# Performance work log

Hardware: AMD Instinct MI355X
Metric: run time of the kernel (lower is better)

Reference implementation:

```python
import jax, jax.numpy as jnp
import numpy as np

L, T, E, D, H, B = 2, 8, 2, 128, 128, 32768
NE = T * E  # total experts per layer = 16


def setup_inputs() -> dict:
    key = jax.random.key(0)
    ks = jax.random.split(key, 8)
    s = 1.0 / np.sqrt(D)
    inputs = jax.random.normal(ks[0], (B, T, D), dtype=jnp.float32)
    w1 = jax.random.uniform(ks[1], (L, NE, D, H), jnp.float32, -s, s)
    b1 = jax.random.uniform(ks[2], (L, NE, H), jnp.float32, -s, s)
    w2 = jax.random.uniform(ks[3], (L, NE, H, H), jnp.float32, -s, s)
    b2 = jax.random.uniform(ks[4], (L, NE, H), jnp.float32, -s, s)
    gate_w = jax.random.uniform(ks[5], (L, T, D, NE), jnp.float32, -s, s)
    gate_b = jax.random.uniform(ks[6], (L, T, NE), jnp.float32, -s, s)
    se = 1.0 / np.sqrt(E)
    sew = jax.random.uniform(ks[7], (L, T, E), jnp.float32, -se, se)
    return {"inputs": inputs, "w1": w1, "b1": b1, "w2": w2, "b2": b2,
            "gate_w": gate_w, "gate_b": gate_b, "sew": sew}


def reference(inputs, w1, b1, w2, b2, gate_w, gate_b, sew):
    x = inputs  # [B, T, D]
    for l in range(L):
        # each task's input feeds its num_task_experts experts
        x_exp = jnp.repeat(x, E, axis=1)  # [B, NE, D]
        h = jax.nn.relu(jnp.einsum('bed,edh->beh', x_exp, w1[l]) + b1[l])
        eo = jax.nn.relu(jnp.einsum('beh,eho->beo', h, w2[l]) + b2[l])  # [B, NE, H]
        # per-task gating over all experts
        gates = jax.nn.softmax(jnp.einsum('btd,tde->bte', x, gate_w[l]) + gate_b[l], axis=-1)  # [B, T, NE]
        fused = jnp.einsum('bte,beh->bth', gates, eo)  # [B, T, H]
        # self-expert residual (num_task_experts > 1 branch)
        eo_r = eo.reshape(eo.shape[0], T, E, -1)  # [B, T, E, H]
        fused = fused + jnp.einsum('te,bteh->bth', sew[l], eo_r)
        x = fused
    return x
```

## Files before the change

### kernel.cpp

```cpp
#include <hip/hip_runtime.h>


typedef float f32x4 __attribute__((ext_vector_type(4)));
typedef _Float16 f16;
typedef f16 f16x8 __attribute__((ext_vector_type(8)));
typedef f16 f16x4 __attribute__((ext_vector_type(4)));

#define MFMA(a, b, c) __builtin_amdgcn_mfma_f32_16x16x32_f16(a, b, c, 0, 0, 0)
#define LOSC (1.0f / 2048.0f)

__device__ __forceinline__ void split2h(float f, f16& h, f16& l) {
  h = (f16)f;
  l = (f16)((f - (float)h) * 2048.0f);
}

__global__ __launch_bounds__(256) void kxform(
    const float* __restrict__ w1, const float* __restrict__ w2,
    const float* __restrict__ gw, f16* __restrict__ w1T,
    f16* __restrict__ w2T, f16* __restrict__ gwT) {
  int idx = blockIdx.x * 256 + threadIdx.x;
  if (idx < 131072) {
    const float* src = (idx < 65536) ? w1 : w2;
    f16* dst = (idx < 65536) ? w1T : w2T;
    int i = idx & 65535;
    int lane = i & 63;
    int it = (i >> 6) & 7;
    int ks = (i >> 9) & 3;
    int q = i >> 11;
    int g = lane >> 4, le = lane & 15;
    f16x8 vh;
#pragma unroll
    for (int j = 0; j < 8; ++j)
      vh[j] = (f16)src[((size_t)q * 128 + (32 * ks + 8 * g + j)) * 128 + 16 * it + le];
    *(f16x8*)(dst + (size_t)i * 8) = vh;
  } else {
    int i = idx - 131072;
    if (i >= 4096) return;
    int lane = i & 63;
    int ks = (i >> 6) & 3;
    int q = (i >> 8) & 15;
    int g = lane >> 4, le = lane & 15;
    f16x8 vh, vl;
#pragma unroll
    for (int j = 0; j < 8; ++j) {
      float f = gw[((size_t)q * 128 + (32 * ks + 8 * g + j)) * 16 + le];
      f16 h, l;
      split2h(f, h, l);
      vh[j] = h;
      vl[j] = l;
    }
    *(f16x8*)(gwT + (size_t)i * 8) = vh;
    *(f16x8*)(gwT + 32768 + (size_t)i * 8) = vl;
  }
}

__global__ __launch_bounds__(256, 2) void kexp(
    const float* __restrict__ x0, const f16* __restrict__ x1in,
    const f16* __restrict__ w1T, const f16* __restrict__ w2T,
    const float* __restrict__ b1, const float* __restrict__ b2,
    f16* __restrict__ eo, int layer) {
  __shared__ f16 sX[2][8192];
  __shared__ f16 sH[8192];
  __shared__ f16 sEO[8192];
  const int tid = threadIdx.x;
  const int lane = tid & 63;
  const int it2 = tid >> 6;
  const int g = lane >> 4, le = lane & 15;
  const int e = blockIdx.x & 15;
  const int r0 = (blockIdx.x >> 4) * 1024;
  const int te = e >> 1;
  const int lx = layer * 16 + e;

  f16x8 w1r[2][4], w2r[2][4];
#pragma unroll
  for (int i2 = 0; i2 < 2; ++i2)
#pragma unroll
    for (int ks = 0; ks < 4; ++ks) {
      size_t fb = ((size_t)((lx * 4 + ks) * 8 + 2 * it2 + i2) * 64 + lane) * 8;
      w1r[i2][ks] = *(const f16x8*)(w1T + fb);
      w2r[i2][ks] = *(const f16x8*)(w2T + fb);
    }
  f32x4 b1v[2], b2v[2];
#pragma unroll
  for (int i2 = 0; i2 < 2; ++i2) {
    b1v[i2] = *(const f32x4*)(b1 + lx * 128 + 32 * it2 + 16 * i2 + 4 * g);
    b2v[i2] = *(const f32x4*)(b2 + lx * 128 + 32 * it2 + 16 * i2 + 4 * g);
  }

  const int srow = tid >> 2;
  const int gr = (tid & 3) * 4;
  f16x8 pre[4];
  auto stage_load = [&](int tile) {
    size_t base = ((size_t)(r0 + tile * 64 + srow) * 8 + te) * 128 + gr * 8;
    if (layer == 0) {
#pragma unroll
      for (int q = 0; q < 4; ++q) {
        f32x4 f0 = *(const f32x4*)(x0 + base + q * 8);
        f32x4 f1 = *(const f32x4*)(x0 + base + q * 8 + 4);
#pragma unroll
        for (int z = 0; z < 4; ++z) {
          pre[q][z] = (f16)f0[z];
          pre[q][4 + z] = (f16)f1[z];
        }
      }
    } else {
#pragma unroll
      for (int q = 0; q < 4; ++q)
        pre[q] = *(const f16x8*)(x1in + base + q * 8);
    }
  };
  auto stage_write = [&](int buf) {
#pragma unroll
    for (int q = 0; q < 4; ++q)
      *(f16x8*)(&sX[buf][srow * 128 + 8 * ((gr + q) ^ (srow & 7))]) = pre[q];
  };
  auto eo_flush = [&](int tile) {
#pragma unroll
    for (int i = 0; i < 4; ++i) {
      int slot = i * 256 + tid;
      int row = slot >> 4, c = slot & 15;
      f16x8 v = *(const f16x8*)(&sEO[row * 128 + 8 * (c ^ (row & 7))]);
      *(f16x8*)(eo + ((size_t)(r0 + tile * 64 + row) * 16 + e) * 128 + 8 * c) = v;
    }
  };

  stage_load(0);
  stage_write(0);
  __syncthreads();

  for (int tile = 0; tile < 16; ++tile) {
    const int b = tile & 1;
    if (tile < 15) stage_load(tile + 1);
    if (tile > 0) eo_flush(tile - 1);
    {
      f32x4 a[2][4];
#pragma unroll
      for (int i2 = 0; i2 < 2; ++i2)
#pragma unroll
        for (int j = 0; j < 4; ++j) a[i2][j] = f32x4{0.f, 0.f, 0.f, 0.f};
#pragma unroll
      for (int ks = 0; ks < 4; ++ks)
#pragma unroll
        for (int j = 0; j < 4; ++j) {
          int brow = 16 * j + le;
          f16x8 bf = *(const f16x8*)(&sX[b][brow * 128 + 8 * ((4 * ks + g) ^ (brow & 7))]);
#pragma unroll
          for (int i2 = 0; i2 < 2; ++i2)
            a[i2][j] = MFMA(w1r[i2][ks], bf, a[i2][j]);
        }
#pragma unroll
      for (int i2 = 0; i2 < 2; ++i2)
#pragma unroll
        for (int j = 0; j < 4; ++j) {
          int brow = 16 * j + le;
          f16x4 hv;
#pragma unroll
          for (int r = 0; r < 4; ++r)
            hv[r] = (f16)fmaxf(a[i2][j][r] + b1v[i2][r], 0.f);
          *(f16x4*)(&sH[brow * 128 + 8 * ((4 * it2 + 2 * i2 + (g >> 1)) ^ (brow & 7)) +
                        4 * (g & 1)]) = hv;
        }
    }
    __syncthreads();
    {
      f32x4 a[2][4];
#pragma unroll
      for (int i2 = 0; i2 < 2; ++i2)
#pragma unroll
        for (int j = 0; j < 4; ++j) a[i2][j] = f32x4{0.f, 0.f, 0.f, 0.f};
#pragma unroll
      for (int ks = 0; ks < 4; ++ks)
#pragma unroll
        for (int j = 0; j < 4; ++j) {
          int brow = 16 * j + le;
          f16x8 bf = *(const f16x8*)(&sH[brow * 128 + 8 * ((4 * ks + g) ^ (brow & 7))]);
#pragma unroll
          for (int i2 = 0; i2 < 2; ++i2)
            a[i2][j] = MFMA(w2r[i2][ks], bf, a[i2][j]);
        }
#pragma unroll
      for (int i2 = 0; i2 < 2; ++i2)
#pragma unroll
        for (int j = 0; j < 4; ++j) {
          int brow = 16 * j + le;
          f16x4 ev;
#pragma unroll
          for (int r = 0; r < 4; ++r)
            ev[r] = (f16)fmaxf(a[i2][j][r] + b2v[i2][r], 0.f);
          *(f16x4*)(&sEO[brow * 128 + 8 * ((4 * it2 + 2 * i2 + (g >> 1)) ^ (brow & 7)) +
                         4 * (g & 1)]) = ev;
        }
    }
    if (tile < 15) stage_write(b ^ 1);
#pragma unroll
    for (int i2 = 0; i2 < 2; ++i2)
#pragma unroll
      for (int ks = 0; ks < 4; ++ks) {
        asm volatile("" : "+v"(w1r[i2][ks]));
        asm volatile("" : "+v"(w2r[i2][ks]));
      }
    __syncthreads();
  }
  eo_flush(15);
}

__global__ __launch_bounds__(512, 4) void kmix(
    const float* __restrict__ x0, const f16* __restrict__ x1in,
    const f16* __restrict__ gwT, const float* __restrict__ gb,
    const float* __restrict__ sw, const f16* __restrict__ eo,
    f16* __restrict__ x1out, float* __restrict__ fout, int layer) {
  __shared__ float sG[8 * 16 * 32];
  const int tid = threadIdx.x;
  const int lane = tid & 63;
  const int t = tid >> 6;
  const int g = lane >> 4, le = lane & 15;
  const int r0 = blockIdx.x * 32;
  const int lt = layer * 8 + t;

  {
    f32x4 l1[2], l2[2];
#pragma unroll
    for (int j = 0; j < 2; ++j) {
      l1[j] = f32x4{0.f, 0.f, 0.f, 0.f};
      l2[j] = f32x4{0.f, 0.f, 0.f, 0.f};
    }
#pragma unroll
    for (int ks = 0; ks < 4; ++ks) {
      size_t fb = ((size_t)(lt * 4 + ks) * 64 + lane) * 8;
      f16x8 ah = *(const f16x8*)(gwT + fb);
      f16x8 al = *(const f16x8*)(gwT + 32768 + fb);
#pragma unroll
      for (int j = 0; j < 2; ++j) {
        size_t xoff = ((size_t)(r0 + 16 * j + le) * 8 + t) * 128 + 32 * ks + 8 * g;
        f16x8 bf;
        if (layer == 0) {
          f32x4 f0 = *(const f32x4*)(x0 + xoff);
          f32x4 f1 = *(const f32x4*)(x0 + xoff + 4);
#pragma unroll
          for (int z = 0; z < 4; ++z) {
            bf[z] = (f16)f0[z];
            bf[4 + z] = (f16)f1[z];
          }
        } else {
          bf = *(const f16x8*)(x1in + xoff);
        }
        l1[j] = MFMA(ah, bf, l1[j]);
        l2[j] = MFMA(al, bf, l2[j]);
      }
    }
#pragma unroll
    for (int j = 0; j < 2; ++j) {
      float zb[4];
#pragma unroll
      for (int r = 0; r < 4; ++r)
        zb[r] = l1[j][r] + l2[j][r] * LOSC + gb[lt * 16 + 4 * g + r];
      float m4 = fmaxf(fmaxf(zb[0], zb[1]), fmaxf(zb[2], zb[3]));
      m4 = fmaxf(m4, __shfl_xor(m4, 16, 64));
      m4 = fmaxf(m4, __shfl_xor(m4, 32, 64));
      float p4[4], s4 = 0.f;
#pragma unroll
      for (int r = 0; r < 4; ++r) {
        p4[r] = __expf(zb[r] - m4);
        s4 += p4[r];
      }
      s4 += __shfl_xor(s4, 16, 64);
      s4 += __shfl_xor(s4, 32, 64);
      float inv = 1.f / s4;
#pragma unroll
      for (int r = 0; r < 4; ++r)
        sG[(t * 16 + 4 * g + r) * 32 + 16 * j + le] = p4[r] * inv;
    }
  }
  __syncthreads();

  const int lrow = tid >> 4;
  const int grow = r0 + lrow;
  const int c0 = (tid & 15) * 8;
  f32x4 am[8][2];
#pragma unroll
  for (int tt = 0; tt < 8; ++tt)
#pragma unroll
    for (int k = 0; k < 2; ++k) am[tt][k] = f32x4{0.f, 0.f, 0.f, 0.f};

  for (int ee = 0; ee < 16; ++ee) {
    const int tte = ee >> 1, eh = ee & 1;
    f16x8 ev = *(const f16x8*)(eo + ((size_t)grow * 16 + ee) * 128 + c0);
    float evf[8];
#pragma unroll
    for (int z = 0; z < 8; ++z) evf[z] = (float)ev[z];
    float ssew = sw[(layer * 8 + tte) * 2 + eh];
#pragma unroll
    for (int tt = 0; tt < 8; ++tt) {
      float coef = sG[(tt * 16 + ee) * 32 + lrow] + (tt == tte ? ssew : 0.f);
#pragma unroll
      for (int z = 0; z < 8; ++z)
        am[tt][z >> 2][z & 3] = fmaf(coef, evf[z], am[tt][z >> 2][z & 3]);
    }
  }
#pragma unroll
  for (int tt = 0; tt < 8; ++tt) {
    size_t off = ((size_t)grow * 8 + tt) * 128 + c0;
    if (layer == 0) {
      f16x8 hv;
#pragma unroll
      for (int z = 0; z < 8; ++z) hv[z] = (f16)am[tt][z >> 2][z & 3];
      *(f16x8*)(x1out + off) = hv;
    } else {
      *(f32x4*)(fout + off) = am[tt][0];
      *(f32x4*)(fout + off + 4) = am[tt][1];
    }
  }
}

extern "C" void kernel_launch(void* const* d_in, const int* in_sizes, int n_in,
                              void* d_out, int out_size, void* d_ws, size_t ws_size,
                              hipStream_t stream) {
  const float* x0 = (const float*)d_in[0];
  const float* w1 = (const float*)d_in[1];
  const float* b1 = (const float*)d_in[2];
  const float* w2 = (const float*)d_in[3];
  const float* b2 = (const float*)d_in[4];
  const float* gw = (const float*)d_in[5];
  const float* gb = (const float*)d_in[6];
  const float* sw = (const float*)d_in[7];

  f16* w1T = (f16*)d_ws;
  f16* w2T = (f16*)((char*)d_ws + 1048576);
  f16* gwT = (f16*)((char*)d_ws + 2097152);
  f16* x1h = (f16*)((char*)d_ws + 4194304);
  f16* eo = (f16*)((char*)d_ws + 71303168);
  float* out = (float*)d_out;

  kxform<<<528, 256, 0, stream>>>(w1, w2, gw, w1T, w2T, gwT);

  kexp<<<512, 256, 0, stream>>>(x0, nullptr, w1T, w2T, b1, b2, eo, 0);
  kmix<<<1024, 512, 0, stream>>>(x0, nullptr, gwT, gb, sw, eo, x1h, nullptr, 0);
  kexp<<<512, 256, 0, stream>>>(nullptr, x1h, w1T, w2T, b1, b2, eo, 1);
  kmix<<<1024, 512, 0, stream>>>(nullptr, x1h, gwT, gb, sw, eo, nullptr, out, 1);
}
```

Measured before the change: 290.5 us.

## Process batch in four chunks and store expert outputs expert-major

The batch is split into four chunks of 8192 rows. Both layers' expert and mixing kernels run per chunk, so the fp16 expert-output buffer written by kexp and read by kmix is a quarter the size and more likely to stay in cache between the two kernels. The eo buffer layout changes from row-major-by-expert to expert-major within a chunk. In exchange there are four times as many kernel launches. Each kexp block now processes only 4 tiles, so its register-resident weight loads are spread over less work, and kmix gets fewer blocks per launch, which may underfill the GPU.

```diff
diff --git a/kernel.cpp b/kernel.cpp
--- a/kernel.cpp
+++ b/kernel.cpp
@@ -8,6 +8,7 @@
 
 #define MFMA(a, b, c) __builtin_amdgcn_mfma_f32_16x16x32_f16(a, b, c, 0, 0, 0)
 #define LOSC (1.0f / 2048.0f)
+#define CH 8192
 
 __device__ __forceinline__ void split2h(float f, f16& h, f16& l) {
   h = (f16)f;
@@ -58,7 +59,7 @@
     const float* __restrict__ x0, const f16* __restrict__ x1in,
     const f16* __restrict__ w1T, const f16* __restrict__ w2T,
     const float* __restrict__ b1, const float* __restrict__ b2,
-    f16* __restrict__ eo, int layer) {
+    f16* __restrict__ eo, int layer, int c0) {
   __shared__ f16 sX[2][8192];
   __shared__ f16 sH[8192];
   __shared__ f16 sEO[8192];
@@ -67,7 +68,7 @@
   const int it2 = tid >> 6;
   const int g = lane >> 4, le = lane & 15;
   const int e = blockIdx.x & 15;
-  const int r0 = (blockIdx.x >> 4) * 1024;
+  const int r0l = (blockIdx.x >> 4) * 256;
   const int te = e >> 1;
   const int lx = layer * 16 + e;
 
@@ -91,7 +92,8 @@
   const int gr = (tid & 3) * 4;
   f16x8 pre[4];
   auto stage_load = [&](int tile) {
-    size_t base = ((size_t)(r0 + tile * 64 + srow) * 8 + te) * 128 + gr * 8;
+    size_t base =
+        ((size_t)(c0 + r0l + tile * 64 + srow) * 8 + te) * 128 + gr * 8;
     if (layer == 0) {
 #pragma unroll
       for (int q = 0; q < 4; ++q) {
@@ -120,7 +122,7 @@
       int slot = i * 256 + tid;
       int row = slot >> 4, c = slot & 15;
       f16x8 v = *(const f16x8*)(&sEO[row * 128 + 8 * (c ^ (row & 7))]);
-      *(f16x8*)(eo + ((size_t)(r0 + tile * 64 + row) * 16 + e) * 128 + 8 * c) = v;
+      *(f16x8*)(eo + ((size_t)e * CH + (r0l + tile * 64 + row)) * 128 + 8 * c) = v;
     }
   };
 
@@ -128,9 +130,9 @@
   stage_write(0);
   __syncthreads();
 
-  for (int tile = 0; tile < 16; ++tile) {
+  for (int tile = 0; tile < 4; ++tile) {
     const int b = tile & 1;
-    if (tile < 15) stage_load(tile + 1);
+    if (tile < 3) stage_load(tile + 1);
     if (tile > 0) eo_flush(tile - 1);
     {
       f32x4 a[2][4];
@@ -191,7 +193,7 @@
                          4 * (g & 1)]) = ev;
         }
     }
-    if (tile < 15) stage_write(b ^ 1);
+    if (tile < 3) stage_write(b ^ 1);
 #pragma unroll
     for (int i2 = 0; i2 < 2; ++i2)
 #pragma unroll
@@ -201,20 +203,20 @@
       }
     __syncthreads();
   }
-  eo_flush(15);
+  eo_flush(3);
 }
 
 __global__ __launch_bounds__(512, 4) void kmix(
     const float* __restrict__ x0, const f16* __restrict__ x1in,
     const f16* __restrict__ gwT, const float* __restrict__ gb,
     const float* __restrict__ sw, const f16* __restrict__ eo,
-    f16* __restrict__ x1out, float* __restrict__ fout, int layer) {
+    f16* __restrict__ x1out, float* __restrict__ fout, int layer, int c0) {
   __shared__ float sG[8 * 16 * 32];
   const int tid = threadIdx.x;
   const int lane = tid & 63;
   const int t = tid >> 6;
   const int g = lane >> 4, le = lane & 15;
-  const int r0 = blockIdx.x * 32;
+  const int lr0 = blockIdx.x * 32;
   const int lt = layer * 8 + t;
 
   {
@@ -231,7 +233,8 @@
       f16x8 al = *(const f16x8*)(gwT + 32768 + fb);
 #pragma unroll
       for (int j = 0; j < 2; ++j) {
-        size_t xoff = ((size_t)(r0 + 16 * j + le) * 8 + t) * 128 + 32 * ks + 8 * g;
+        size_t xoff =
+            ((size_t)(c0 + lr0 + 16 * j + le) * 8 + t) * 128 + 32 * ks + 8 * g;
         f16x8 bf;
         if (layer == 0) {
           f32x4 f0 = *(const f32x4*)(x0 + xoff);
@@ -274,8 +277,9 @@
   __syncthreads();
 
   const int lrow = tid >> 4;
-  const int grow = r0 + lrow;
-  const int c0 = (tid & 15) * 8;
+  const int lr = lr0 + lrow;
+  const int grow = c0 + lr;
+  const int cq = (tid & 15) * 8;
   f32x4 am[8][2];
 #pragma unroll
   for (int tt = 0; tt < 8; ++tt)
@@ -284,7 +288,7 @@
 
   for (int ee = 0; ee < 16; ++ee) {
     const int tte = ee >> 1, eh = ee & 1;
-    f16x8 ev = *(const f16x8*)(eo + ((size_t)grow * 16 + ee) * 128 + c0);
+    f16x8 ev = *(const f16x8*)(eo + ((size_t)ee * CH + lr) * 128 + cq);
     float evf[8];
 #pragma unroll
     for (int z = 0; z < 8; ++z) evf[z] = (float)ev[z];
@@ -299,7 +303,7 @@
   }
 #pragma unroll
   for (int tt = 0; tt < 8; ++tt) {
-    size_t off = ((size_t)grow * 8 + tt) * 128 + c0;
+    size_t off = ((size_t)grow * 8 + tt) * 128 + cq;
     if (layer == 0) {
       f16x8 hv;
 #pragma unroll
@@ -333,8 +337,11 @@
 
   kxform<<<528, 256, 0, stream>>>(w1, w2, gw, w1T, w2T, gwT);
 
-  kexp<<<512, 256, 0, stream>>>(x0, nullptr, w1T, w2T, b1, b2, eo, 0);
-  kmix<<<1024, 512, 0, stream>>>(x0, nullptr, gwT, gb, sw, eo, x1h, nullptr, 0);
-  kexp<<<512, 256, 0, stream>>>(nullptr, x1h, w1T, w2T, b1, b2, eo, 1);
-  kmix<<<1024, 512, 0, stream>>>(nullptr, x1h, gwT, gb, sw, eo, nullptr, out, 1);
-}
+  for (int c = 0; c < 4; ++c) {
+    int c0 = c * CH;
+    kexp<<<512, 256, 0, stream>>>(x0, x1h, w1T, w2T, b1, b2, eo, 0, c0);
+    kmix<<<256, 512, 0, stream>>>(x0, x1h, gwT, gb, sw, eo, x1h, out, 0, c0);
+    kexp<<<512, 256, 0, stream>>>(x0, x1h, w1T, w2T, b1, b2, eo, 1, c0);
+    kmix<<<256, 512, 0, stream>>>(x0, x1h, gwT, gb, sw, eo, nullptr, out, 1, c0);
+  }
+}
```

New measurement: 312.0 us. 1.07x slower.

## Pre-cast input to fp16 and stage expert tiles via direct global-to-LDS loads

Applied to the files above, without the earlier changes.

Adds a separate cast kernel that converts the fp32 input to fp16 once, so both layer-0 kernels read half-precision data instead of each converting fp32 on the fly. The expert kernel now fills its shared-memory input tiles with global_load_lds (direct global-to-LDS copies with a swizzled source), which removes the register prefetch buffer and the separate LDS write step. The expert-output buffer layout changes from row-major per batch to per-expert contiguous. The trade-off is an extra pass over the input and a larger workspace footprint.

```diff
diff --git a/kernel.cpp b/kernel.cpp
--- a/kernel.cpp
+++ b/kernel.cpp
@@ -8,10 +8,26 @@
 
 #define MFMA(a, b, c) __builtin_amdgcn_mfma_f32_16x16x32_f16(a, b, c, 0, 0, 0)
 #define LOSC (1.0f / 2048.0f)
+#define AS1 __attribute__((address_space(1)))
+#define AS3 __attribute__((address_space(3)))
 
 __device__ __forceinline__ void split2h(float f, f16& h, f16& l) {
   h = (f16)f;
   l = (f16)((f - (float)h) * 2048.0f);
+}
+
+__global__ __launch_bounds__(256) void kxcast(const float* __restrict__ x0,
+                                              f16* __restrict__ x0h) {
+  size_t i = ((size_t)blockIdx.x * 256 + threadIdx.x) * 8;
+  f32x4 f0 = *(const f32x4*)(x0 + i);
+  f32x4 f1 = *(const f32x4*)(x0 + i + 4);
+  f16x8 v;
+#pragma unroll
+  for (int z = 0; z < 4; ++z) {
+    v[z] = (f16)f0[z];
+    v[4 + z] = (f16)f1[z];
+  }
+  *(f16x8*)(x0h + i) = v;
 }
 
 __global__ __launch_bounds__(256) void kxform(
@@ -55,10 +71,9 @@
 }
 
 __global__ __launch_bounds__(256, 2) void kexp(
-    const float* __restrict__ x0, const f16* __restrict__ x1in,
-    const f16* __restrict__ w1T, const f16* __restrict__ w2T,
-    const float* __restrict__ b1, const float* __restrict__ b2,
-    f16* __restrict__ eo, int layer) {
+    const f16* __restrict__ xs, const f16* __restrict__ w1T,
+    const f16* __restrict__ w2T, const float* __restrict__ b1,
+    const float* __restrict__ b2, f16* __restrict__ eo, int layer) {
   __shared__ f16 sX[2][8192];
   __shared__ f16 sH[8192];
   __shared__ f16 sEO[8192];
@@ -87,32 +102,17 @@
     b2v[i2] = *(const f32x4*)(b2 + lx * 128 + 32 * it2 + 16 * i2 + 4 * g);
   }
 
-  const int srow = tid >> 2;
-  const int gr = (tid & 3) * 4;
-  f16x8 pre[4];
-  auto stage_load = [&](int tile) {
-    size_t base = ((size_t)(r0 + tile * 64 + srow) * 8 + te) * 128 + gr * 8;
-    if (layer == 0) {
-#pragma unroll
-      for (int q = 0; q < 4; ++q) {
-        f32x4 f0 = *(const f32x4*)(x0 + base + q * 8);
-        f32x4 f1 = *(const f32x4*)(x0 + base + q * 8 + 4);
-#pragma unroll
-        for (int z = 0; z < 4; ++z) {
-          pre[q][z] = (f16)f0[z];
-          pre[q][4 + z] = (f16)f1[z];
-        }
-      }
-    } else {
-#pragma unroll
-      for (int q = 0; q < 4; ++q)
-        pre[q] = *(const f16x8*)(x1in + base + q * 8);
-    }
-  };
-  auto stage_write = [&](int buf) {
-#pragma unroll
-    for (int q = 0; q < 4; ++q)
-      *(f16x8*)(&sX[buf][srow * 128 + 8 * ((gr + q) ^ (srow & 7))]) = pre[q];
+  auto stage_gl = [&](int buf, int tile) {
+#pragma unroll
+    for (int i = 0; i < 4; ++i) {
+      int row = 16 * it2 + 4 * i + (lane >> 4);
+      int gc = lane & 15;
+      const f16* src = xs + ((size_t)(r0 + tile * 64 + row) * 8 + te) * 128 +
+                       (gc ^ (row & 7)) * 8;
+      f16* dst = &sX[buf][(16 * it2 + 4 * i) * 128];
+      __builtin_amdgcn_global_load_lds((const AS1 void*)src, (AS3 void*)dst,
+                                       16, 0, 0);
+    }
   };
   auto eo_flush = [&](int tile) {
 #pragma unroll
@@ -120,17 +120,16 @@
       int slot = i * 256 + tid;
       int row = slot >> 4, c = slot & 15;
       f16x8 v = *(const f16x8*)(&sEO[row * 128 + 8 * (c ^ (row & 7))]);
-      *(f16x8*)(eo + ((size_t)(r0 + tile * 64 + row) * 16 + e) * 128 + 8 * c) = v;
+      *(f16x8*)(eo + ((size_t)e * 32768 + (r0 + tile * 64 + row)) * 128 + 8 * c) = v;
     }
   };
 
-  stage_load(0);
-  stage_write(0);
+  stage_gl(0, 0);
   __syncthreads();
 
   for (int tile = 0; tile < 16; ++tile) {
     const int b = tile & 1;
-    if (tile < 15) stage_load(tile + 1);
+    if (tile < 15) stage_gl(b ^ 1, tile + 1);
     if (tile > 0) eo_flush(tile - 1);
     {
       f32x4 a[2][4];
@@ -191,24 +190,16 @@
                          4 * (g & 1)]) = ev;
         }
     }
-    if (tile < 15) stage_write(b ^ 1);
-#pragma unroll
-    for (int i2 = 0; i2 < 2; ++i2)
-#pragma unroll
-      for (int ks = 0; ks < 4; ++ks) {
-        asm volatile("" : "+v"(w1r[i2][ks]));
-        asm volatile("" : "+v"(w2r[i2][ks]));
-      }
     __syncthreads();
   }
   eo_flush(15);
 }
 
 __global__ __launch_bounds__(512, 4) void kmix(
-    const float* __restrict__ x0, const f16* __restrict__ x1in,
-    const f16* __restrict__ gwT, const float* __restrict__ gb,
-    const float* __restrict__ sw, const f16* __restrict__ eo,
-    f16* __restrict__ x1out, float* __restrict__ fout, int layer) {
+    const f16* __restrict__ xs, const f16* __restrict__ gwT,
+    const float* __restrict__ gb, const float* __restrict__ sw,
+    const f16* __restrict__ eo, f16* __restrict__ x1out,
+    float* __restrict__ fout, int layer) {
   __shared__ float sG[8 * 16 * 32];
   const int tid = threadIdx.x;
   const int lane = tid & 63;
@@ -231,19 +222,8 @@
       f16x8 al = *(const f16x8*)(gwT + 32768 + fb);
 #pragma unroll
       for (int j = 0; j < 2; ++j) {
-        size_t xoff = ((size_t)(r0 + 16 * j + le) * 8 + t) * 128 + 32 * ks + 8 * g;
-        f16x8 bf;
-        if (layer == 0) {
-          f32x4 f0 = *(const f32x4*)(x0 + xoff);
-          f32x4 f1 = *(const f32x4*)(x0 + xoff + 4);
-#pragma unroll
-          for (int z = 0; z < 4; ++z) {
-            bf[z] = (f16)f0[z];
-            bf[4 + z] = (f16)f1[z];
-          }
-        } else {
-          bf = *(const f16x8*)(x1in + xoff);
-        }
+        f16x8 bf = *(const f16x8*)(xs + ((size_t)(r0 + 16 * j + le) * 8 + t) * 128 +
+                                   32 * ks + 8 * g);
         l1[j] = MFMA(ah, bf, l1[j]);
         l2[j] = MFMA(al, bf, l2[j]);
       }
@@ -275,7 +255,7 @@
 
   const int lrow = tid >> 4;
   const int grow = r0 + lrow;
-  const int c0 = (tid & 15) * 8;
+  const int cq = (tid & 15) * 8;
   f32x4 am[8][2];
 #pragma unroll
   for (int tt = 0; tt < 8; ++tt)
@@ -284,7 +264,7 @@
 
   for (int ee = 0; ee < 16; ++ee) {
     const int tte = ee >> 1, eh = ee & 1;
-    f16x8 ev = *(const f16x8*)(eo + ((size_t)grow * 16 + ee) * 128 + c0);
+    f16x8 ev = *(const f16x8*)(eo + ((size_t)ee * 32768 + grow) * 128 + cq);
     float evf[8];
 #pragma unroll
     for (int z = 0; z < 8; ++z) evf[z] = (float)ev[z];
@@ -299,7 +279,7 @@
   }
 #pragma unroll
   for (int tt = 0; tt < 8; ++tt) {
-    size_t off = ((size_t)grow * 8 + tt) * 128 + c0;
+    size_t off = ((size_t)grow * 8 + tt) * 128 + cq;
     if (layer == 0) {
       f16x8 hv;
 #pragma unroll
@@ -327,14 +307,16 @@
   f16* w1T = (f16*)d_ws;
   f16* w2T = (f16*)((char*)d_ws + 1048576);
   f16* gwT = (f16*)((char*)d_ws + 2097152);
-  f16* x1h = (f16*)((char*)d_ws + 4194304);
-  f16* eo = (f16*)((char*)d_ws + 71303168);
+  f16* x0h = (f16*)((char*)d_ws + 4194304);
+  f16* x1h = (f16*)((char*)d_ws + 71303168);
+  f16* eo = (f16*)((char*)d_ws + 138412032);
   float* out = (float*)d_out;
 
   kxform<<<528, 256, 0, stream>>>(w1, w2, gw, w1T, w2T, gwT);
-
-  kexp<<<512, 256, 0, stream>>>(x0, nullptr, w1T, w2T, b1, b2, eo, 0);
-  kmix<<<1024, 512, 0, stream>>>(x0, nullptr, gwT, gb, sw, eo, x1h, nullptr, 0);
-  kexp<<<512, 256, 0, stream>>>(nullptr, x1h, w1T, w2T, b1, b2, eo, 1);
-  kmix<<<1024, 512, 0, stream>>>(nullptr, x1h, gwT, gb, sw, eo, nullptr, out, 1);
-}
+  kxcast<<<16384, 256, 0, stream>>>(x0, x0h);
+
+  kexp<<<512, 256, 0, stream>>>(x0h, w1T, w2T, b1, b2, eo, 0);
+  kmix<<<1024, 512, 0, stream>>>(x0h, gwT, gb, sw, eo, x1h, nullptr, 0);
+  kexp<<<512, 256, 0, stream>>>(x1h, w1T, w2T, b1, b2, eo, 1);
+  kmix<<<1024, 512, 0, stream>>>(x1h, gwT, gb, sw, eo, nullptr, out, 1);
+}
```

Measured after the change: 275.7 us. 1.05x faster.
